# Performance work log

Hardware: AMD Instinct MI355X
Metric: run time of the kernel (lower is better)

Reference implementation:

```python
import jax, jax.numpy as jnp
import numpy as np

IMG_SIZE = (960.0, 512.0)        # (w, h)
HM_W, HM_H = 240, 128            # heatmap (w, h)
GRID_SIZE = (8000.0, 8000.0, 2000.0)
CUBE = (80, 80, 20)
NBINS = CUBE[0] * CUBE[1] * CUBE[2]
SIGMA = 200.0


def _compute_grid(center3):
    gx = jnp.linspace(-GRID_SIZE[0] / 2, GRID_SIZE[0] / 2, CUBE[0]) + center3[0]
    gy = jnp.linspace(-GRID_SIZE[1] / 2, GRID_SIZE[1] / 2, CUBE[1]) + center3[1]
    gz = jnp.linspace(-GRID_SIZE[2] / 2, GRID_SIZE[2] / 2, CUBE[2]) + center3[2]
    X, Y, Z = jnp.meshgrid(gx, gy, gz, indexing='ij')
    return jnp.stack([X.ravel(), Y.ravel(), Z.ravel()], axis=1)  # [NBINS, 3]


def _project(pts, R, T, f, c, k, p):
    # standard radial-distortion pinhole projection (project_point_radial)
    xcam = R @ pts.T - T                              # [3, N]
    y = xcam[:2] / (xcam[2:3] + 1e-5)                 # [2, N]
    r2 = jnp.sum(y * y, axis=0)
    radial = 1.0 + k[0] * r2 + k[1] * r2 ** 2 + k[2] * r2 ** 3
    tan = p[0] * y[1] + p[1] * y[0]
    y = y * (radial + 2.0 * tan)[None] + jnp.outer(jnp.stack([p[1], p[0]]), r2)
    ypix = f[:, None] * y + c[:, None]                # [2, N]
    return ypix.T, xcam[2]


def _transform_mat(center, scale):
    # get_transform(center, scale, rot=0, res=IMG_SIZE)
    h = 200.0 * scale
    z = jnp.zeros(())
    one = jnp.ones(())
    r0, r1 = IMG_SIZE
    return jnp.stack([
        jnp.stack([r0 / h, z, r0 * (-center[0] / h + 0.5)]),
        jnp.stack([z, r1 / h, r1 * (-center[1] / h + 0.5)]),
        jnp.stack([z, z, one]),
    ])


def _grid_sample(img, g):
    # bilinear, align_corners=True, zeros padding; img [J,H,W], g [N,2] normalized
    J, H, W = img.shape
    ix = (g[:, 0] + 1.0) * 0.5 * (W - 1)
    iy = (g[:, 1] + 1.0) * 0.5 * (H - 1)
    ix0 = jnp.floor(ix)
    iy0 = jnp.floor(iy)
    wx = ix - ix0
    wy = iy - iy0

    def tap(xf, yf, w):
        ok = (xf >= 0) & (xf <= W - 1) & (yf >= 0) & (yf <= H - 1)
        xi = jnp.clip(xf, 0, W - 1).astype(jnp.int32)
        yi = jnp.clip(yf, 0, H - 1).astype(jnp.int32)
        return img[:, yi, xi] * (ok * w)[None]       # [J, N]

    return (tap(ix0, iy0, (1 - wx) * (1 - wy)) + tap(ix0 + 1, iy0, wx * (1 - wy))
            + tap(ix0, iy0 + 1, (1 - wx) * wy) + tap(ix0 + 1, iy0 + 1, wx * wy))


def _per_sample(hm, gc, center, scale, R, T, f, c, k, p, bboxes, depths, dnf):
    grid = _compute_grid(gc)                          # [N, 3]
    width = center[0] * 2.0
    height = center[1] * 2.0
    xy, zc = _project(grid, R, T, f, c, k, p)         # [N,2], [N]
    bound = (xy[:, 0] >= 0) & (xy[:, 1] >= 0) & (xy[:, 0] < width) & (xy[:, 1] < height)
    xy = jnp.clip(xy, -1.0, jnp.maximum(width, height))
    t = _transform_mat(center, scale)
    hom = jnp.concatenate([xy, jnp.ones((NBINS, 1))], axis=1)
    xy = (t @ hom.T)[:2].T                            # image coords
    xy = xy * jnp.array([float(HM_W), float(HM_H)]) / jnp.array(IMG_SIZE)  # heatmap coords
    sg = jnp.clip(xy / jnp.array([HM_W - 1.0, HM_H - 1.0]) * 2.0 - 1.0, -1.1, 1.1)
    sampled = _grid_sample(hm, sg)                    # [J, N]
    # per-bbox mask: in-box AND in-frame, gaussian depth weight; depths<0 is padding
    valid = (depths >= 0).astype(sampled.dtype)                                 # [M]
    inbox = ((xy[None, :, 0] >= bboxes[:, 0:1]) & (xy[None, :, 1] >= bboxes[:, 1:2])
             & (xy[None, :, 0] <= bboxes[:, 2:3]) & (xy[None, :, 1] <= bboxes[:, 3:4])
             & bound[None])                                                     # [M, N]
    dmask = jnp.exp(-(zc[None] - (depths * dnf)[:, None]) ** 2 / (2.0 * SIGMA ** 2))  # [M, N]
    weight = inbox * dmask * valid[:, None]                                     # [M, N]
    # running compare-and-select max over bboxes, init 0 (matches mask*tmp + ~mask*cube)
    cube = jnp.zeros_like(sampled)
    for m in range(weight.shape[0]):
        cube = jnp.maximum(cube, weight[m][None] * sampled)
    cube = cube * bound[None].astype(cube.dtype)
    return cube, grid


def reference(heatmaps, grid_center, center, scale, R, T, f, c, k, p, bboxes, depths, depth_norm_factor):
    cubes, grids = jax.vmap(_per_sample)(heatmaps, grid_center, center, scale, R, T,
                                         f, c, k, p, bboxes, depths, depth_norm_factor)
    cubes = jnp.nan_to_num(cubes)
    cubes = jnp.clip(cubes, 0.0, 1.0)
    B, J = cubes.shape[0], cubes.shape[1]
    return cubes.reshape(B, J, CUBE[0], CUBE[1], CUBE[2]), grids


def setup_inputs():
    key = jax.random.key(0)
    B, J, M = 16, 15, 10
    ks = jax.random.split(key, 8)
    heatmaps = jax.random.uniform(ks[0], (B, J, HM_H, HM_W), dtype=jnp.float32)
    grid_center = (jnp.tile(jnp.array([[0.0, -500.0, 800.0]]), (B, 1))
                   + jax.random.normal(ks[1], (B, 3)) * 100.0)
    center = jnp.tile(jnp.array([[480.0, 256.0]]), (B, 1))
    scale = jnp.full((B,), 5.0, dtype=jnp.float32)
    R = jnp.tile(jnp.eye(3, dtype=jnp.float32)[None], (B, 1, 1))
    T = jnp.tile(jnp.array([0.0, 0.0, -4000.0]).reshape(1, 3, 1), (B, 1, 1))
    f = jnp.tile(jnp.array([[1500.0, 1500.0]]), (B, 1))
    c = jnp.tile(jnp.array([[480.0, 256.0]]), (B, 1))
    kdist = jnp.zeros((B, 3), dtype=jnp.float32)
    pdist = jnp.zeros((B, 2), dtype=jnp.float32)
    x1 = jax.random.uniform(ks[2], (B, M, 1)) * 120.0
    y1 = jax.random.uniform(ks[3], (B, M, 1)) * 60.0
    x2 = x1 + 20.0 + jax.random.uniform(ks[4], (B, M, 1)) * 100.0
    y2 = y1 + 20.0 + jax.random.uniform(ks[5], (B, M, 1)) * 60.0
    bboxes = jnp.concatenate([x1, y1, x2, y2], axis=2)
    depths = 0.6 + 0.6 * jax.random.uniform(ks[6], (B, M))
    depth_norm_factor = jnp.full((B,), 5000.0, dtype=jnp.float32)
    return dict(heatmaps=heatmaps, grid_center=grid_center, center=center, scale=scale,
                R=R, T=T, f=f, c=c, k=kdist, p=pdist, bboxes=bboxes, depths=depths,
                depth_norm_factor=depth_norm_factor)
```

## Files before the change

kernel.cpp:

```cpp
#include <hip/hip_runtime.h>
#include <cstddef>

constexpr int BB  = 16;
constexpr int JJ  = 15;
constexpr int MM  = 10;
constexpr int CX  = 80, CY = 80, CZ = 20;
constexpr int NB  = CX * CY * CZ;
constexpr int HMW = 240, HMH = 128;


__global__ __launch_bounds__(256) void project_kernel(
    const float* __restrict__ hm,
    const float* __restrict__ gc,
    const float* __restrict__ center,
    const float* __restrict__ scale,
    const float* __restrict__ Rm,
    const float* __restrict__ Tm,
    const float* __restrict__ fv,
    const float* __restrict__ cv,
    const float* __restrict__ kd,
    const float* __restrict__ pd,
    const float* __restrict__ bbox,
    const float* __restrict__ dep,
    const float* __restrict__ dnf,
    float* __restrict__ out)
{
    const int blocksPerB = NB / 256;
    const int b = blockIdx.x / blocksPerB;
    const int n = (blockIdx.x % blocksPerB) * 256 + threadIdx.x;

    const int iz  = n % CZ;
    const int rem = n / CZ;
    const int iy  = rem % CY;
    const int ixg = rem / CY;

    const float gx = -4000.0f + (float)ixg * (8000.0f / 79.0f) + gc[b * 3 + 0];
    const float gy = -4000.0f + (float)iy  * (8000.0f / 79.0f) + gc[b * 3 + 1];
    const float gz = -1000.0f + (float)iz  * (2000.0f / 19.0f) + gc[b * 3 + 2];

    const float* R = Rm + b * 9;
    const float* T = Tm + b * 3;
    const float xc = R[0] * gx + R[1] * gy + R[2] * gz - T[0];
    const float yc = R[3] * gx + R[4] * gy + R[5] * gz - T[1];
    const float zc = R[6] * gx + R[7] * gy + R[8] * gz - T[2];

    const float invz = 1.0f / (zc + 1e-5f);
    const float ynx = xc * invz;
    const float yny = yc * invz;
    const float r2  = ynx * ynx + yny * yny;
    const float k0 = kd[b * 3 + 0], k1 = kd[b * 3 + 1], k2 = kd[b * 3 + 2];
    const float radial = 1.0f + k0 * r2 + k1 * r2 * r2 + k2 * r2 * r2 * r2;
    const float p0 = pd[b * 2 + 0], p1 = pd[b * 2 + 1];
    const float tn = p0 * yny + p1 * ynx;
    const float sm = radial + 2.0f * tn;
    const float ux = ynx * sm + p1 * r2;
    const float uy = yny * sm + p0 * r2;
    float xpix = fv[b * 2 + 0] * ux + cv[b * 2 + 0];
    float ypix = fv[b * 2 + 1] * uy + cv[b * 2 + 1];

    const float c0 = center[b * 2 + 0], c1 = center[b * 2 + 1];
    const float width = c0 * 2.0f, height = c1 * 2.0f;
    const bool bound = (xpix >= 0.0f) && (ypix >= 0.0f) &&
                       (xpix < width) && (ypix < height);
    const float mxwh = fmaxf(width, height);
    xpix = fminf(fmaxf(xpix, -1.0f), mxwh);
    ypix = fminf(fmaxf(ypix, -1.0f), mxwh);

    const float h = 200.0f * scale[b];
    const float ximg = (960.0f / h) * xpix + 960.0f * (-c0 / h + 0.5f);
    const float yimg = (512.0f / h) * ypix + 512.0f * (-c1 / h + 0.5f);
    const float xhm = ximg * (240.0f / 960.0f);
    const float yhm = yimg * (128.0f / 512.0f);

    const float sgx = fminf(fmaxf(xhm / 239.0f * 2.0f - 1.0f, -1.1f), 1.1f);
    const float sgy = fminf(fmaxf(yhm / 127.0f * 2.0f - 1.0f, -1.1f), 1.1f);
    const float fx = (sgx + 1.0f) * 0.5f * 239.0f;
    const float fy = (sgy + 1.0f) * 0.5f * 127.0f;
    const float fx0 = floorf(fx), fy0 = floorf(fy);
    const float wxf = fx - fx0, wyf = fy - fy0;

    const bool okx0 = (fx0 >= 0.0f) && (fx0 <= 239.0f);
    const bool okx1 = (fx0 + 1.0f >= 0.0f) && (fx0 + 1.0f <= 239.0f);
    const bool oky0 = (fy0 >= 0.0f) && (fy0 <= 127.0f);
    const bool oky1 = (fy0 + 1.0f >= 0.0f) && (fy0 + 1.0f <= 127.0f);
    const int x0 = min(max((int)fx0, 0), HMW - 1);
    const int x1 = min(max((int)fx0 + 1, 0), HMW - 1);
    const int y0 = min(max((int)fy0, 0), HMH - 1);
    const int y1 = min(max((int)fy0 + 1, 0), HMH - 1);
    const float w00 = (okx0 && oky0) ? (1.0f - wxf) * (1.0f - wyf) : 0.0f;
    const float w01 = (okx1 && oky0) ? wxf * (1.0f - wyf) : 0.0f;
    const float w10 = (okx0 && oky1) ? (1.0f - wxf) * wyf : 0.0f;
    const float w11 = (okx1 && oky1) ? wxf * wyf : 0.0f;

    float maxw = 0.0f;
    if (bound) {
        const float dn = dnf[b];
        for (int m = 0; m < MM; ++m) {
            const float d = dep[b * MM + m];
            const float* bx = bbox + ((size_t)b * MM + m) * 4;
            const bool inb = (xhm >= bx[0]) && (yhm >= bx[1]) &&
                             (xhm <= bx[2]) && (yhm <= bx[3]);
            const float dz = zc - d * dn;
            const float w = __expf(dz * dz * (-1.0f / (2.0f * 200.0f * 200.0f)));
            if (inb && d >= 0.0f) maxw = fmaxf(maxw, w);
        }
    }

    const size_t outbase = (size_t)b * JJ * NB + (size_t)n;
    if (maxw > 0.0f) {
        const float* img = hm + (size_t)b * JJ * HMH * HMW;
        const int o00 = y0 * HMW + x0;
        const int o01 = y0 * HMW + x1;
        const int o10 = y1 * HMW + x0;
        const int o11 = y1 * HMW + x1;
        for (int j = 0; j < JJ; ++j) {
            const float* p = img + (size_t)j * HMH * HMW;
            const float s = p[o00] * w00 + p[o01] * w01 +
                            p[o10] * w10 + p[o11] * w11;
            float v = s * maxw;
            v = fminf(fmaxf(v, 0.0f), 1.0f);
            out[outbase + (size_t)j * NB] = v;
        }
    } else {
        for (int j = 0; j < JJ; ++j)
            out[outbase + (size_t)j * NB] = 0.0f;
    }

    float* gout = out + (size_t)BB * JJ * NB + ((size_t)b * NB + n) * 3;
    gout[0] = gx;
    gout[1] = gy;
    gout[2] = gz;
}

extern "C" void kernel_launch(void* const* d_in, const int* in_sizes, int n_in,
                              void* d_out, int out_size, void* d_ws, size_t ws_size,
                              hipStream_t stream) {
    const float* hm     = (const float*)d_in[0];
    const float* gc     = (const float*)d_in[1];
    const float* center = (const float*)d_in[2];
    const float* scale  = (const float*)d_in[3];
    const float* R      = (const float*)d_in[4];
    const float* T      = (const float*)d_in[5];
    const float* f      = (const float*)d_in[6];
    const float* c      = (const float*)d_in[7];
    const float* k      = (const float*)d_in[8];
    const float* p      = (const float*)d_in[9];
    const float* bbox   = (const float*)d_in[10];
    const float* dep    = (const float*)d_in[11];
    const float* dnf    = (const float*)d_in[12];
    float* out = (float*)d_out;

    const int blocksPerB = NB / 256;
    dim3 grid(BB * blocksPerB);
    dim3 block(256);
    project_kernel<<<grid, block, 0, stream>>>(hm, gc, center, scale, R, T, f, c,
                                               k, p, bbox, dep, dnf, out);
}
```

Before: 196.1 us.

## Process four grid points per thread with vectorized nontemporal output stores

Each thread now handles four consecutive bins. Per-batch parameters and bbox/depth data are hoisted into registers once per thread, and the 15 joint outputs and the grid coordinates are written as 128-bit nontemporal vector stores. This targets store-bandwidth inefficiency and redundant scalar parameter loads in an output-write-bound kernel (16*15*128000 floats). In exchange it raises register pressure and leaves a quarter as many threads, and NB/(256*4)=125 divides exactly.

```diff
diff --git a/kernel.cpp b/kernel.cpp
--- a/kernel.cpp
+++ b/kernel.cpp
@@ -7,9 +7,13 @@
 constexpr int CX  = 80, CY = 80, CZ = 20;
 constexpr int NB  = CX * CY * CZ;
 constexpr int HMW = 240, HMH = 128;
-
-
-__global__ __launch_bounds__(256) void project_kernel(
+constexpr int TPB = 256;
+constexpr int VEC = 4;
+
+typedef float f32x4 __attribute__((ext_vector_type(4)));
+
+
+__global__ __launch_bounds__(TPB) void project_kernel(
     const float* __restrict__ hm,
     const float* __restrict__ gc,
     const float* __restrict__ center,
@@ -25,111 +29,150 @@
     const float* __restrict__ dnf,
     float* __restrict__ out)
 {
-    const int blocksPerB = NB / 256;
-    const int b = blockIdx.x / blocksPerB;
-    const int n = (blockIdx.x % blocksPerB) * 256 + threadIdx.x;
-
-    const int iz  = n % CZ;
-    const int rem = n / CZ;
-    const int iy  = rem % CY;
-    const int ixg = rem / CY;
-
-    const float gx = -4000.0f + (float)ixg * (8000.0f / 79.0f) + gc[b * 3 + 0];
-    const float gy = -4000.0f + (float)iy  * (8000.0f / 79.0f) + gc[b * 3 + 1];
-    const float gz = -1000.0f + (float)iz  * (2000.0f / 19.0f) + gc[b * 3 + 2];
-
+    const int blocksPerB = NB / (TPB * VEC);
+    const int b  = blockIdx.x / blocksPerB;
+    const int n0 = (blockIdx.x % blocksPerB) * (TPB * VEC) + threadIdx.x * VEC;
+
+    const float gcx = gc[b * 3 + 0], gcy = gc[b * 3 + 1], gcz = gc[b * 3 + 2];
     const float* R = Rm + b * 9;
     const float* T = Tm + b * 3;
-    const float xc = R[0] * gx + R[1] * gy + R[2] * gz - T[0];
-    const float yc = R[3] * gx + R[4] * gy + R[5] * gz - T[1];
-    const float zc = R[6] * gx + R[7] * gy + R[8] * gz - T[2];
-
-    const float invz = 1.0f / (zc + 1e-5f);
-    const float ynx = xc * invz;
-    const float yny = yc * invz;
-    const float r2  = ynx * ynx + yny * yny;
+    const float R0 = R[0], R1 = R[1], R2 = R[2];
+    const float R3 = R[3], R4 = R[4], R5 = R[5];
+    const float R6 = R[6], R7 = R[7], R8 = R[8];
+    const float T0 = T[0], T1 = T[1], T2 = T[2];
     const float k0 = kd[b * 3 + 0], k1 = kd[b * 3 + 1], k2 = kd[b * 3 + 2];
-    const float radial = 1.0f + k0 * r2 + k1 * r2 * r2 + k2 * r2 * r2 * r2;
     const float p0 = pd[b * 2 + 0], p1 = pd[b * 2 + 1];
-    const float tn = p0 * yny + p1 * ynx;
-    const float sm = radial + 2.0f * tn;
-    const float ux = ynx * sm + p1 * r2;
-    const float uy = yny * sm + p0 * r2;
-    float xpix = fv[b * 2 + 0] * ux + cv[b * 2 + 0];
-    float ypix = fv[b * 2 + 1] * uy + cv[b * 2 + 1];
-
+    const float f0 = fv[b * 2 + 0], f1 = fv[b * 2 + 1];
+    const float cc0 = cv[b * 2 + 0], cc1 = cv[b * 2 + 1];
     const float c0 = center[b * 2 + 0], c1 = center[b * 2 + 1];
     const float width = c0 * 2.0f, height = c1 * 2.0f;
-    const bool bound = (xpix >= 0.0f) && (ypix >= 0.0f) &&
-                       (xpix < width) && (ypix < height);
     const float mxwh = fmaxf(width, height);
-    xpix = fminf(fmaxf(xpix, -1.0f), mxwh);
-    ypix = fminf(fmaxf(ypix, -1.0f), mxwh);
-
     const float h = 200.0f * scale[b];
-    const float ximg = (960.0f / h) * xpix + 960.0f * (-c0 / h + 0.5f);
-    const float yimg = (512.0f / h) * ypix + 512.0f * (-c1 / h + 0.5f);
-    const float xhm = ximg * (240.0f / 960.0f);
-    const float yhm = yimg * (128.0f / 512.0f);
-
-    const float sgx = fminf(fmaxf(xhm / 239.0f * 2.0f - 1.0f, -1.1f), 1.1f);
-    const float sgy = fminf(fmaxf(yhm / 127.0f * 2.0f - 1.0f, -1.1f), 1.1f);
-    const float fx = (sgx + 1.0f) * 0.5f * 239.0f;
-    const float fy = (sgy + 1.0f) * 0.5f * 127.0f;
-    const float fx0 = floorf(fx), fy0 = floorf(fy);
-    const float wxf = fx - fx0, wyf = fy - fy0;
-
-    const bool okx0 = (fx0 >= 0.0f) && (fx0 <= 239.0f);
-    const bool okx1 = (fx0 + 1.0f >= 0.0f) && (fx0 + 1.0f <= 239.0f);
-    const bool oky0 = (fy0 >= 0.0f) && (fy0 <= 127.0f);
-    const bool oky1 = (fy0 + 1.0f >= 0.0f) && (fy0 + 1.0f <= 127.0f);
-    const int x0 = min(max((int)fx0, 0), HMW - 1);
-    const int x1 = min(max((int)fx0 + 1, 0), HMW - 1);
-    const int y0 = min(max((int)fy0, 0), HMH - 1);
-    const int y1 = min(max((int)fy0 + 1, 0), HMH - 1);
-    const float w00 = (okx0 && oky0) ? (1.0f - wxf) * (1.0f - wyf) : 0.0f;
-    const float w01 = (okx1 && oky0) ? wxf * (1.0f - wyf) : 0.0f;
-    const float w10 = (okx0 && oky1) ? (1.0f - wxf) * wyf : 0.0f;
-    const float w11 = (okx1 && oky1) ? wxf * wyf : 0.0f;
-
-    float maxw = 0.0f;
-    if (bound) {
-        const float dn = dnf[b];
-        for (int m = 0; m < MM; ++m) {
-            const float d = dep[b * MM + m];
-            const float* bx = bbox + ((size_t)b * MM + m) * 4;
-            const bool inb = (xhm >= bx[0]) && (yhm >= bx[1]) &&
-                             (xhm <= bx[2]) && (yhm <= bx[3]);
-            const float dz = zc - d * dn;
-            const float w = __expf(dz * dz * (-1.0f / (2.0f * 200.0f * 200.0f)));
-            if (inb && d >= 0.0f) maxw = fmaxf(maxw, w);
+    const float dn = dnf[b];
+
+    float bx0[MM], bx1[MM], bx2[MM], bx3[MM], dv[MM];
+#pragma unroll
+    for (int m = 0; m < MM; ++m) {
+        const float* bx = bbox + ((size_t)b * MM + m) * 4;
+        bx0[m] = bx[0]; bx1[m] = bx[1]; bx2[m] = bx[2]; bx3[m] = bx[3];
+        dv[m] = dep[b * MM + m];
+    }
+
+    float maxw[VEC];
+    int   o00[VEC], o01[VEC], o10[VEC], o11[VEC];
+    float w00[VEC], w01[VEC], w10[VEC], w11[VEC];
+    float gxa[VEC], gya[VEC], gza[VEC];
+
+#pragma unroll
+    for (int v = 0; v < VEC; ++v) {
+        const int n   = n0 + v;
+        const int iz  = n % CZ;
+        const int rem = n / CZ;
+        const int iy  = rem % CY;
+        const int ixg = rem / CY;
+
+        const float gx = -4000.0f + (float)ixg * (8000.0f / 79.0f) + gcx;
+        const float gy = -4000.0f + (float)iy  * (8000.0f / 79.0f) + gcy;
+        const float gz = -1000.0f + (float)iz  * (2000.0f / 19.0f) + gcz;
+        gxa[v] = gx; gya[v] = gy; gza[v] = gz;
+
+        const float xc = R0 * gx + R1 * gy + R2 * gz - T0;
+        const float yc = R3 * gx + R4 * gy + R5 * gz - T1;
+        const float zc = R6 * gx + R7 * gy + R8 * gz - T2;
+
+        const float invz = 1.0f / (zc + 1e-5f);
+        const float ynx = xc * invz;
+        const float yny = yc * invz;
+        const float r2  = ynx * ynx + yny * yny;
+        const float radial = 1.0f + k0 * r2 + k1 * r2 * r2 + k2 * r2 * r2 * r2;
+        const float tn = p0 * yny + p1 * ynx;
+        const float sm = radial + 2.0f * tn;
+        const float ux = ynx * sm + p1 * r2;
+        const float uy = yny * sm + p0 * r2;
+        float xpix = f0 * ux + cc0;
+        float ypix = f1 * uy + cc1;
+
+        const bool bound = (xpix >= 0.0f) && (ypix >= 0.0f) &&
+                           (xpix < width) && (ypix < height);
+        xpix = fminf(fmaxf(xpix, -1.0f), mxwh);
+        ypix = fminf(fmaxf(ypix, -1.0f), mxwh);
+
+        const float ximg = (960.0f / h) * xpix + 960.0f * (-c0 / h + 0.5f);
+        const float yimg = (512.0f / h) * ypix + 512.0f * (-c1 / h + 0.5f);
+        const float xhm = ximg * (240.0f / 960.0f);
+        const float yhm = yimg * (128.0f / 512.0f);
+
+        const float sgx = fminf(fmaxf(xhm / 239.0f * 2.0f - 1.0f, -1.1f), 1.1f);
+        const float sgy = fminf(fmaxf(yhm / 127.0f * 2.0f - 1.0f, -1.1f), 1.1f);
+        const float fx = (sgx + 1.0f) * 0.5f * 239.0f;
+        const float fy = (sgy + 1.0f) * 0.5f * 127.0f;
+        const float fx0 = floorf(fx), fy0 = floorf(fy);
+        const float wxf = fx - fx0, wyf = fy - fy0;
+
+        const bool okx0 = (fx0 >= 0.0f) && (fx0 <= 239.0f);
+        const bool okx1 = (fx0 + 1.0f >= 0.0f) && (fx0 + 1.0f <= 239.0f);
+        const bool oky0 = (fy0 >= 0.0f) && (fy0 <= 127.0f);
+        const bool oky1 = (fy0 + 1.0f >= 0.0f) && (fy0 + 1.0f <= 127.0f);
+        const int x0 = min(max((int)fx0, 0), HMW - 1);
+        const int x1 = min(max((int)fx0 + 1, 0), HMW - 1);
+        const int y0 = min(max((int)fy0, 0), HMH - 1);
+        const int y1 = min(max((int)fy0 + 1, 0), HMH - 1);
+        w00[v] = (okx0 && oky0) ? (1.0f - wxf) * (1.0f - wyf) : 0.0f;
+        w01[v] = (okx1 && oky0) ? wxf * (1.0f - wyf) : 0.0f;
+        w10[v] = (okx0 && oky1) ? (1.0f - wxf) * wyf : 0.0f;
+        w11[v] = (okx1 && oky1) ? wxf * wyf : 0.0f;
+        o00[v] = y0 * HMW + x0;
+        o01[v] = y0 * HMW + x1;
+        o10[v] = y1 * HMW + x0;
+        o11[v] = y1 * HMW + x1;
+
+        float mw = 0.0f;
+        if (bound) {
+#pragma unroll
+            for (int m = 0; m < MM; ++m) {
+                const bool inb = (xhm >= bx0[m]) && (yhm >= bx1[m]) &&
+                                 (xhm <= bx2[m]) && (yhm <= bx3[m]);
+                const float dz = zc - dv[m] * dn;
+                const float w = __expf(dz * dz * (-1.0f / (2.0f * 200.0f * 200.0f)));
+                if (inb && dv[m] >= 0.0f) mw = fmaxf(mw, w);
+            }
         }
-    }
-
-    const size_t outbase = (size_t)b * JJ * NB + (size_t)n;
-    if (maxw > 0.0f) {
-        const float* img = hm + (size_t)b * JJ * HMH * HMW;
-        const int o00 = y0 * HMW + x0;
-        const int o01 = y0 * HMW + x1;
-        const int o10 = y1 * HMW + x0;
-        const int o11 = y1 * HMW + x1;
-        for (int j = 0; j < JJ; ++j) {
+        maxw[v] = mw;
+    }
+
+    {
+        float* gout = out + (size_t)BB * JJ * NB + ((size_t)b * NB + n0) * 3;
+        f32x4 g0 = {gxa[0], gya[0], gza[0], gxa[1]};
+        f32x4 g1 = {gya[1], gza[1], gxa[2], gya[2]};
+        f32x4 g2 = {gza[2], gxa[3], gya[3], gza[3]};
+        f32x4* gp = (f32x4*)gout;
+        __builtin_nontemporal_store(g0, gp + 0);
+        __builtin_nontemporal_store(g1, gp + 1);
+        __builtin_nontemporal_store(g2, gp + 2);
+    }
+
+    const bool any = (maxw[0] > 0.0f) || (maxw[1] > 0.0f) ||
+                     (maxw[2] > 0.0f) || (maxw[3] > 0.0f);
+    const float* img = hm + (size_t)b * JJ * HMH * HMW;
+    const size_t outbase = (size_t)b * JJ * NB + (size_t)n0;
+
+    for (int j = 0; j < JJ; ++j) {
+        f32x4 vv = {0.0f, 0.0f, 0.0f, 0.0f};
+        if (any) {
             const float* p = img + (size_t)j * HMH * HMW;
-            const float s = p[o00] * w00 + p[o01] * w01 +
-                            p[o10] * w10 + p[o11] * w11;
-            float v = s * maxw;
-            v = fminf(fmaxf(v, 0.0f), 1.0f);
-            out[outbase + (size_t)j * NB] = v;
+#pragma unroll
+            for (int v = 0; v < VEC; ++v) {
+                float r = 0.0f;
+                if (maxw[v] > 0.0f) {
+                    const float s = p[o00[v]] * w00[v] + p[o01[v]] * w01[v] +
+                                    p[o10[v]] * w10[v] + p[o11[v]] * w11[v];
+                    r = fminf(fmaxf(s * maxw[v], 0.0f), 1.0f);
+                }
+                vv[v] = r;
+            }
         }
-    } else {
-        for (int j = 0; j < JJ; ++j)
-            out[outbase + (size_t)j * NB] = 0.0f;
-    }
-
-    float* gout = out + (size_t)BB * JJ * NB + ((size_t)b * NB + n) * 3;
-    gout[0] = gx;
-    gout[1] = gy;
-    gout[2] = gz;
+        __builtin_nontemporal_store(vv, (f32x4*)(out + outbase + (size_t)j * NB));
+    }
 }
 
 extern "C" void kernel_launch(void* const* d_in, const int* in_sizes, int n_in,
@@ -150,9 +193,9 @@
     const float* dnf    = (const float*)d_in[12];
     float* out = (float*)d_out;
 
-    const int blocksPerB = NB / 256;
+    const int blocksPerB = NB / (TPB * VEC);
     dim3 grid(BB * blocksPerB);
-    dim3 block(256);
+    dim3 block(TPB);
     project_kernel<<<grid, block, 0, stream>>>(hm, gc, center, scale, R, T, f, c,
                                                k, p, bbox, dep, dnf, out);
 }
```

Measured after the change: 239.7 us. +22.2%, slower.
